# Kernel optimization log

Hardware: AMD Instinct MI355X
Metric: run time of the kernel (lower is better)

## Reference

```python
import jax, jax.numpy as jnp
import numpy as np

ALPHA = 0.2  # LeakyReLU negative slope


def setup_inputs() -> dict:
    key = jax.random.key(0)
    k1, k2, k3, k4 = jax.random.split(key, 4)
    B, N, Fin, Fout = 8, 2048, 256, 256
    h = jax.random.normal(k1, (B, N, Fin), dtype=jnp.float32)
    # random 0/1 adjacency with guaranteed self-loops so every row has a neighbor
    adj = jax.random.randint(k2, (N, N), 0, 2).astype(jnp.float32)
    adj = jnp.maximum(adj, jnp.eye(N, dtype=jnp.float32))
    # xavier_uniform with gain=1.414
    def xavier(k, shape, gain=1.414):
        fan_in, fan_out = shape[0], shape[1]
        a = gain * np.sqrt(6.0 / (fan_in + fan_out))
        return jax.random.uniform(k, shape, dtype=jnp.float32, minval=-a, maxval=a)
    W = xavier(k3, (Fin, Fout))
    a = xavier(k4, (2 * Fout, 1))
    return {"h": h, "adj_matrix": adj, "W": W, "a": a}


def reference(h, adj_matrix, W, a):
    # h: [B, N, Fin], adj_matrix: [N, N], W: [Fin, Fout], a: [2*Fout, 1]
    Fout = W.shape[1]
    Wh = jnp.einsum("bnf,fo->bno", h, W)            # [B, N, Fout]
    a1, a2 = a[:Fout, 0], a[Fout:, 0]                 # split additive attention vector
    # e[b,i,j] = leakyrelu(Wh[b,i]@a1 + Wh[b,j]@a2) — equals concat([Wh_i,Wh_j])@a
    s1 = Wh @ a1                                      # [B, N]
    s2 = Wh @ a2                                      # [B, N]
    e = s1[:, :, None] + s2[:, None, :]               # [B, N, N]
    e = jnp.where(e >= 0, e, ALPHA * e)               # LeakyReLU
    e = jnp.where(adj_matrix[None] == 0, -jnp.inf, e)  # mask non-edges
    attention = jax.nn.softmax(e, axis=-1)            # [B, N, N]
    # dropout is identity in eval mode (training=False)
    h_prime = jnp.einsum("bij,bjo->bio", attention, Wh)
    return h_prime
```

## Files before the change

### kernel.cpp

```cpp
#include <hip/hip_runtime.h>
#include <cstdint>

#define NN 2048
#define LOG2E 1.4426950408889634f

typedef __attribute__((ext_vector_type(8))) short bf16x8;
typedef __attribute__((ext_vector_type(4))) float f32x4;

__device__ __forceinline__ unsigned short f2bf(float x){
  union { float f; unsigned u; } v; v.f = x;
  unsigned r = v.u + 0x7FFFu + ((v.u >> 16) & 1u);
  return (unsigned short)(r >> 16);
}
__device__ __forceinline__ unsigned pack2(float a, float b){
  return (unsigned)f2bf(a) | ((unsigned)f2bf(b) << 16);
}
__device__ __forceinline__ unsigned permpack(unsigned hi, unsigned lo){
  return __builtin_amdgcn_perm(hi, lo, 0x07060302u);
}

__global__ __launch_bounds__(256) void k_prep(const float* __restrict__ adj,
                                              const float* __restrict__ W,
                                              unsigned long long* __restrict__ ab,
                                              unsigned short* __restrict__ Wt){
  const int tid = threadIdx.x;
  const int bid = blockIdx.x;
  if (bid < 512){
    const int lane = tid & 63;
    unsigned* ab32 = (unsigned*)ab;
    #pragma unroll
    for (int r = 0; r < 4; r++){
      const int row = bid * 4 + r;
      #pragma unroll
      for (int part = 0; part < 2; part++){
        float4 v = ((const float4*)(adj + (size_t)row * NN))[part * 256 + tid];
        unsigned n = (v.x != 0.f ? 1u : 0u) | (v.y != 0.f ? 2u : 0u)
                   | (v.z != 0.f ? 4u : 0u) | (v.w != 0.f ? 8u : 0u);
        unsigned m;
        m = __shfl_xor(n, 1); n = (lane & 1) ? (m | (n << 4))  : (n | (m << 4));
        m = __shfl_xor(n, 2); n = (lane & 2) ? (m | (n << 8))  : (n | (m << 8));
        m = __shfl_xor(n, 4); n = (lane & 4) ? (m | (n << 16)) : (n | (m << 16));
        if ((lane & 7) == 0)
          ab32[row * 64 + part * 32 + (tid >> 3)] = n;
      }
    }
  } else {
    int g = (bid - 512) * 256 + tid;
    int o = g >> 8, k = g & 255;
    Wt[g] = f2bf(W[k * 256 + o]);
  }
}

__global__ __launch_bounds__(512, 2) void k_fused_gemm(const float* __restrict__ h,
                                                       const unsigned short* __restrict__ Wt,
                                                       const float* __restrict__ a,
                                                       unsigned short* __restrict__ WhT,
                                                       float* __restrict__ s1c,
                                                       float* __restrict__ s2c){
  __shared__ __align__(16) unsigned char As[2 * 8192];
  __shared__ __align__(16) unsigned short Ts[256 * 72];
  __shared__ float s1p[8][64], s2p[8][64];
  const int tid = threadIdx.x;
  const int r0 = blockIdx.x * 64;
  const int b  = r0 >> 11;
  const int i0 = r0 & (NN - 1);
  const int w = tid >> 6, lane = tid & 63, lhi = lane >> 4, llo = lane & 15;
  const int wc = w * 32;
  const int sit = w >> 1, skk = w & 1;
  const int srow = sit * 16 + llo;
  const int skol = skk * 32 + lhi * 8;

  f32x4 acc[4][2];
  #pragma unroll
  for (int i = 0; i < 4; i++)
    #pragma unroll
    for (int j = 0; j < 2; j++){ acc[i][j][0]=0.f; acc[i][j][1]=0.f; acc[i][j][2]=0.f; acc[i][j][3]=0.f; }

  float4 hv[4][2];
  #pragma unroll
  for (int t = 0; t < 4; t++){
    const float* hp = h + (size_t)(r0 + srow) * 256 + t * 64 + skol;
    hv[t][0] = *(const float4*)hp;
    hv[t][1] = *(const float4*)(hp + 4);
  }

  auto loadB = [&](int k0, bf16x8* dst){
    #pragma unroll
    for (int ot = 0; ot < 2; ot++)
      #pragma unroll
      for (int kk = 0; kk < 2; kk++)
        dst[ot * 2 + kk] = *(const bf16x8*)(Wt + (size_t)(wc + ot * 16 + llo) * 256 + k0 + kk * 32 + lhi * 8);
  };
  bf16x8 bfr[2][4];
  loadB(0, bfr[0]);

  #pragma unroll
  for (int t = 0; t < 4; t++){
    uint4 q = make_uint4(pack2(hv[t][0].x, hv[t][0].y), pack2(hv[t][0].z, hv[t][0].w),
                         pack2(hv[t][1].x, hv[t][1].y), pack2(hv[t][1].z, hv[t][1].w));
    *(uint4*)&As[(t & 1) * 8192 + w * 1024 + lane * 16] = q;
    __syncthreads();
    if (t < 3) loadB((t + 1) * 64, bfr[(t + 1) & 1]);
    bf16x8 af[2][4];
    #pragma unroll
    for (int kk = 0; kk < 2; kk++)
      #pragma unroll
      for (int it = 0; it < 4; it++)
        af[kk][it] = *(const bf16x8*)&As[(t & 1) * 8192 + (it * 2 + kk) * 1024 + lane * 16];
    #pragma unroll
    for (int kk = 0; kk < 2; kk++)
      #pragma unroll
      for (int it = 0; it < 4; it++)
        #pragma unroll
        for (int ot = 0; ot < 2; ot++)
          acc[it][ot] = __builtin_amdgcn_mfma_f32_16x16x32_bf16(af[kk][it], bfr[t & 1][ot * 2 + kk], acc[it][ot], 0, 0, 0);
  }

  float a1v[2], a2v[2];
  #pragma unroll
  for (int ot = 0; ot < 2; ot++){
    a1v[ot] = a[wc + ot * 16 + llo] * LOG2E;
    a2v[ot] = a[256 + wc + ot * 16 + llo] * LOG2E;
  }
  #pragma unroll
  for (int it = 0; it < 4; it++){
    #pragma unroll
    for (int q = 0; q < 4; q++){
      float p1 = acc[it][0][q] * a1v[0] + acc[it][1][q] * a1v[1];
      float p2 = acc[it][0][q] * a2v[0] + acc[it][1][q] * a2v[1];
      #pragma unroll
      for (int o = 1; o < 16; o <<= 1){ p1 += __shfl_xor(p1, o); p2 += __shfl_xor(p2, o); }
      if (llo == 0){
        s1p[w][it * 16 + lhi * 4 + q] = p1;
        s2p[w][it * 16 + lhi * 4 + q] = p2;
      }
    }
  }

  #pragma unroll
  for (int it = 0; it < 4; it++){
    #pragma unroll
    for (int ot = 0; ot < 2; ot++){
      int o = wc + ot * 16 + llo;
      uint2 u = make_uint2(pack2(acc[it][ot][0], acc[it][ot][1]),
                           pack2(acc[it][ot][2], acc[it][ot][3]));
      *(uint2*)&Ts[o * 72 + it * 16 + lhi * 4] = u;
    }
  }
  __syncthreads();

  if (tid < 64){
    float t1 = 0.f, t2 = 0.f;
    #pragma unroll
    for (int g = 0; g < 8; g++){ t1 += s1p[g][tid]; t2 += s2p[g][tid]; }
    s1c[r0 + tid] = t1;
    s2c[r0 + tid] = t2;
  }
  #pragma unroll
  for (int p = 0; p < 4; p++){
    int o = p * 64 + (tid >> 3), col = (tid & 7) * 8;
    *(uint4*)(WhT + (size_t)(b * 256 + o) * 2048 + i0 + col) = *(const uint4*)&Ts[o * 72 + col];
  }
}

__global__ __launch_bounds__(512, 2) void k_attn(const float* __restrict__ s1c,
                                                 const float* __restrict__ s2c,
                                                 const unsigned short* __restrict__ WhT,
                                                 const unsigned long long* __restrict__ ab,
                                                 float* __restrict__ out){
  __shared__ __align__(16) float s2s[2048];
  __shared__ __align__(16) unsigned char PsB[2 * 16384];
  __shared__ __align__(16) unsigned char bitsB[64 * 264];
  __shared__ float s1s[64], lin[64], red[8], rsp[8][64];
  const int tid = threadIdx.x;
  const int bid = blockIdx.x;
  const int b = bid & 7, i0 = (bid >> 3) * 64;
  const int w = tid >> 6, lane = tid & 63, lhi = lane >> 4, llo = lane & 15;
  const int wc = w * 32;
  const int sit = w >> 1, skk = w & 1;
  const int sfrag = sit * 2 + skk;
  const int prow = sit * 16 + llo;

  float4 v = ((const float4*)(s2c + (size_t)b * NN))[tid];
  ((float4*)s2s)[tid] = v;
  float vmax = fmaxf(fmaxf(v.x, v.y), fmaxf(v.z, v.w));
  #pragma unroll
  for (int o = 32; o; o >>= 1) vmax = fmaxf(vmax, __shfl_xor(vmax, o));
  if (lane == 0) red[w] = vmax;
  if (tid < 64) s1s[tid] = s1c[(size_t)b * NN + i0 + tid];
  #pragma unroll
  for (int k = 0; k < 4; k++){
    int g = k * 512 + tid;
    unsigned long long mw = ab[(size_t)i0 * 32 + g];
    *(unsigned long long*)&bitsB[(g >> 5) * 264 + (g & 31) * 8] = mw;
  }
  __syncthreads();
  float m2 = red[0];
  #pragma unroll
  for (int g = 1; g < 8; g++) m2 = fmaxf(m2, red[g]);

  const float s1v = s1s[prow];
  const float xm = s1v + m2;
  const float mv = fmaxf(xm, 0.2f * xm);
  const float c1 = s1v - mv;
  const float c2 = 0.2f * s1v - mv;
  float rs = 0.f;

  f32x4 acc[4][2];
  #pragma unroll
  for (int i = 0; i < 4; i++)
    #pragma unroll
    for (int j = 0; j < 2; j++){ acc[i][j][0]=0.f; acc[i][j][1]=0.f; acc[i][j][2]=0.f; acc[i][j][3]=0.f; }

  auto loadB = [&](int j0, bf16x8* dst){
    #pragma unroll
    for (int jh = 0; jh < 2; jh++)
      #pragma unroll
      for (int ot = 0; ot < 2; ot++)
        #pragma unroll
        for (int kk = 0; kk < 2; kk++)
          dst[jh * 4 + ot * 2 + kk] = *(const bf16x8*)(WhT + (size_t)(b * 256 + wc + ot * 16 + llo) * 2048 + j0 + jh * 64 + kk * 32 + lhi * 8);
  };

  unsigned puq[8];
  auto computeP = [&](int tn, unsigned* pq){
    unsigned bits = bitsB[prow * 264 + tn * 8 + skk * 4 + lhi];
    const float* sp = &s2s[tn * 64 + skk * 32 + lhi * 8];
    float4 xa = *(const float4*)sp;
    float4 xb = *(const float4*)(sp + 4);
    float xs[8] = {xa.x, xa.y, xa.z, xa.w, xb.x, xb.y, xb.z, xb.w};
    unsigned pu[8];
    #pragma unroll
    for (int e = 0; e < 8; e++){
      float s2v = xs[e];
      float y = fmaxf(s2v + c1, __builtin_fmaf(0.2f, s2v, c2));
      float p = __builtin_amdgcn_exp2f(y);
      unsigned m = ((bits >> e) & 1u) ? 0xFFFF0000u : 0u;
      unsigned u = __float_as_uint(p) & m;
      rs += __uint_as_float(u);
      pu[e] = u;
    }
    pq[0] = permpack(pu[1], pu[0]); pq[1] = permpack(pu[3], pu[2]);
    pq[2] = permpack(pu[5], pu[4]); pq[3] = permpack(pu[7], pu[6]);
  };

  auto stageBody = [&](int t, int BUF, bf16x8* curB, bf16x8* nxtB, bool last){
    *(uint4*)&PsB[BUF * 16384 +        sfrag * 1024 + lane * 16] = *(uint4*)&puq[0];
    *(uint4*)&PsB[BUF * 16384 + 8192 + sfrag * 1024 + lane * 16] = *(uint4*)&puq[4];
    __syncthreads();
    if (!last) loadB((t + 1) * 128, nxtB);
    bf16x8 af[2][4];
    #pragma unroll
    for (int kk = 0; kk < 2; kk++)
      #pragma unroll
      for (int it = 0; it < 4; it++)
        af[kk][it] = *(const bf16x8*)&PsB[BUF * 16384 + (it * 2 + kk) * 1024 + lane * 16];
    if (!last) computeP(2 * (t + 1), &puq[0]);
    #pragma unroll
    for (int kk = 0; kk < 2; kk++)
      #pragma unroll
      for (int it = 0; it < 4; it++)
        #pragma unroll
        for (int ot = 0; ot < 2; ot++)
          acc[it][ot] = __builtin_amdgcn_mfma_f32_16x16x32_bf16(af[kk][it], curB[ot * 2 + kk], acc[it][ot], 0, 0, 0);
    #pragma unroll
    for (int kk = 0; kk < 2; kk++)
      #pragma unroll
      for (int it = 0; it < 4; it++)
        af[kk][it] = *(const bf16x8*)&PsB[BUF * 16384 + 8192 + (it * 2 + kk) * 1024 + lane * 16];
    if (!last) computeP(2 * (t + 1) + 1, &puq[4]);
    #pragma unroll
    for (int kk = 0; kk < 2; kk++)
      #pragma unroll
      for (int it = 0; it < 4; it++)
        #pragma unroll
        for (int ot = 0; ot < 2; ot++)
          acc[it][ot] = __builtin_amdgcn_mfma_f32_16x16x32_bf16(af[kk][it], curB[4 + ot * 2 + kk], acc[it][ot], 0, 0, 0);
  };

  bf16x8 bA[8], bB[8];
  loadB(0, bA);
  computeP(0, &puq[0]);
  computeP(1, &puq[4]);
  for (int t2 = 0; t2 < 16; t2 += 2){
    stageBody(t2,     0, bA, bB, false);
    stageBody(t2 + 1, 1, bB, bA, t2 + 1 == 15);
  }

  rs += __shfl_xor(rs, 16);
  rs += __shfl_xor(rs, 32);
  if (lhi == 0) rsp[w][prow] = rs;
  __syncthreads();
  if (tid < 64){
    int it = tid >> 4;
    lin[tid] = 1.0f / (rsp[it * 2][tid] + rsp[it * 2 + 1][tid]);
  }
  __syncthreads();

  #pragma unroll
  for (int it = 0; it < 4; it++){
    #pragma unroll
    for (int ot = 0; ot < 2; ot++){
      int col = wc + ot * 16 + llo;
      #pragma unroll
      for (int q = 0; q < 4; q++){
        int row = it * 16 + lhi * 4 + q;
        out[(size_t)(b * NN + i0 + row) * 256 + col] = acc[it][ot][q] * lin[row];
      }
    }
  }
}

extern "C" void kernel_launch(void* const* d_in, const int* in_sizes, int n_in,
                              void* d_out, int out_size, void* d_ws, size_t ws_size,
                              hipStream_t stream) {
  const float* h   = (const float*)d_in[0];
  const float* adj = (const float*)d_in[1];
  const float* W   = (const float*)d_in[2];
  const float* a   = (const float*)d_in[3];
  float* out = (float*)d_out;

  char* ws = (char*)d_ws;
  unsigned short* WhT      = (unsigned short*)(ws);
  unsigned short* Wt       = (unsigned short*)(ws + 8388608);
  unsigned long long* ab   = (unsigned long long*)(ws + 8519680);
  float* s1c               = (float*)(ws + 9043968);
  float* s2c               = (float*)(ws + 9109504);

  hipLaunchKernelGGL(k_prep,       dim3(768), dim3(256), 0, stream, adj, W, ab, Wt);
  hipLaunchKernelGGL(k_fused_gemm, dim3(256), dim3(512), 0, stream, h, Wt, a, WhT, s1c, s2c);
  hipLaunchKernelGGL(k_attn,       dim3(256), dim3(512), 0, stream, s1c, s2c, WhT, ab, out);
}
```

Before: 130.7 us.

## Split attention block across 16 waves, each owning 16 output columns

Doubles the k_attn block from 512 to 1024 threads. Each wave now owns a 16-column output slice instead of 32, and computes only one P fragment per stage instead of two. Row sums are reduced across four wave partials. This halves per-wave accumulator and B-register use and spreads the exp/mask work over more waves to raise latency hiding. In exchange, each wave issues more shared-memory A-fragment reads per MFMA, and barrier cost grows with more waves per block.

```diff
diff --git a/kernel.cpp b/kernel.cpp
--- a/kernel.cpp
+++ b/kernel.cpp
@@ -163,34 +163,35 @@
   }
 }
 
-__global__ __launch_bounds__(512, 2) void k_attn(const float* __restrict__ s1c,
-                                                 const float* __restrict__ s2c,
-                                                 const unsigned short* __restrict__ WhT,
-                                                 const unsigned long long* __restrict__ ab,
-                                                 float* __restrict__ out){
+__global__ __launch_bounds__(1024, 4) void k_attn(const float* __restrict__ s1c,
+                                                  const float* __restrict__ s2c,
+                                                  const unsigned short* __restrict__ WhT,
+                                                  const unsigned long long* __restrict__ ab,
+                                                  float* __restrict__ out){
   __shared__ __align__(16) float s2s[2048];
   __shared__ __align__(16) unsigned char PsB[2 * 16384];
   __shared__ __align__(16) unsigned char bitsB[64 * 264];
-  __shared__ float s1s[64], lin[64], red[8], rsp[8][64];
+  __shared__ float s1s[64], lin[64], red[8], rsp[16][64];
   const int tid = threadIdx.x;
   const int bid = blockIdx.x;
   const int b = bid & 7, i0 = (bid >> 3) * 64;
   const int w = tid >> 6, lane = tid & 63, lhi = lane >> 4, llo = lane & 15;
-  const int wc = w * 32;
-  const int sit = w >> 1, skk = w & 1;
-  const int sfrag = sit * 2 + skk;
-  const int prow = sit * 16 + llo;
-
-  float4 v = ((const float4*)(s2c + (size_t)b * NN))[tid];
-  ((float4*)s2s)[tid] = v;
-  float vmax = fmaxf(fmaxf(v.x, v.y), fmaxf(v.z, v.w));
-  #pragma unroll
-  for (int o = 32; o; o >>= 1) vmax = fmaxf(vmax, __shfl_xor(vmax, o));
-  if (lane == 0) red[w] = vmax;
+  const int wcol = w * 16;
+  const int jh = w >> 3, it = (w >> 1) & 3, kk = w & 1;
+  const int prow = it * 16 + llo;
+
+  if (tid < 512){
+    float4 v = ((const float4*)(s2c + (size_t)b * NN))[tid];
+    ((float4*)s2s)[tid] = v;
+    float vmax = fmaxf(fmaxf(v.x, v.y), fmaxf(v.z, v.w));
+    #pragma unroll
+    for (int o = 32; o; o >>= 1) vmax = fmaxf(vmax, __shfl_xor(vmax, o));
+    if (lane == 0) red[w] = vmax;
+  }
   if (tid < 64) s1s[tid] = s1c[(size_t)b * NN + i0 + tid];
   #pragma unroll
-  for (int k = 0; k < 4; k++){
-    int g = k * 512 + tid;
+  for (int k = 0; k < 2; k++){
+    int g = k * 1024 + tid;
     unsigned long long mw = ab[(size_t)i0 * 32 + g];
     *(unsigned long long*)&bitsB[(g >> 5) * 264 + (g & 31) * 8] = mw;
   }
@@ -206,26 +207,23 @@
   const float c2 = 0.2f * s1v - mv;
   float rs = 0.f;
 
-  f32x4 acc[4][2];
-  #pragma unroll
-  for (int i = 0; i < 4; i++)
-    #pragma unroll
-    for (int j = 0; j < 2; j++){ acc[i][j][0]=0.f; acc[i][j][1]=0.f; acc[i][j][2]=0.f; acc[i][j][3]=0.f; }
+  f32x4 acc[4];
+  #pragma unroll
+  for (int i = 0; i < 4; i++){ acc[i][0]=0.f; acc[i][1]=0.f; acc[i][2]=0.f; acc[i][3]=0.f; }
 
   auto loadB = [&](int j0, bf16x8* dst){
     #pragma unroll
-    for (int jh = 0; jh < 2; jh++)
-      #pragma unroll
-      for (int ot = 0; ot < 2; ot++)
-        #pragma unroll
-        for (int kk = 0; kk < 2; kk++)
-          dst[jh * 4 + ot * 2 + kk] = *(const bf16x8*)(WhT + (size_t)(b * 256 + wc + ot * 16 + llo) * 2048 + j0 + jh * 64 + kk * 32 + lhi * 8);
+    for (int jh2 = 0; jh2 < 2; jh2++)
+      #pragma unroll
+      for (int kk2 = 0; kk2 < 2; kk2++)
+        dst[jh2 * 2 + kk2] = *(const bf16x8*)(WhT + (size_t)(b * 256 + wcol + llo) * 2048 + j0 + jh2 * 64 + kk2 * 32 + lhi * 8);
   };
 
-  unsigned puq[8];
-  auto computeP = [&](int tn, unsigned* pq){
-    unsigned bits = bitsB[prow * 264 + tn * 8 + skk * 4 + lhi];
-    const float* sp = &s2s[tn * 64 + skk * 32 + lhi * 8];
+  unsigned puq[4];
+  auto computeP = [&](int t){
+    int tn = 2 * t + jh;
+    unsigned bits = bitsB[prow * 264 + tn * 8 + kk * 4 + lhi];
+    const float* sp = &s2s[tn * 64 + kk * 32 + lhi * 8];
     float4 xa = *(const float4*)sp;
     float4 xb = *(const float4*)(sp + 4);
     float xs[8] = {xa.x, xa.y, xa.z, xa.w, xb.x, xb.y, xb.z, xb.w};
@@ -240,48 +238,41 @@
       rs += __uint_as_float(u);
       pu[e] = u;
     }
-    pq[0] = permpack(pu[1], pu[0]); pq[1] = permpack(pu[3], pu[2]);
-    pq[2] = permpack(pu[5], pu[4]); pq[3] = permpack(pu[7], pu[6]);
+    puq[0] = permpack(pu[1], pu[0]); puq[1] = permpack(pu[3], pu[2]);
+    puq[2] = permpack(pu[5], pu[4]); puq[3] = permpack(pu[7], pu[6]);
   };
 
   auto stageBody = [&](int t, int BUF, bf16x8* curB, bf16x8* nxtB, bool last){
-    *(uint4*)&PsB[BUF * 16384 +        sfrag * 1024 + lane * 16] = *(uint4*)&puq[0];
-    *(uint4*)&PsB[BUF * 16384 + 8192 + sfrag * 1024 + lane * 16] = *(uint4*)&puq[4];
+    *(uint4*)&PsB[BUF * 16384 + w * 1024 + lane * 16] = *(uint4*)&puq[0];
     __syncthreads();
     if (!last) loadB((t + 1) * 128, nxtB);
     bf16x8 af[2][4];
     #pragma unroll
-    for (int kk = 0; kk < 2; kk++)
-      #pragma unroll
-      for (int it = 0; it < 4; it++)
-        af[kk][it] = *(const bf16x8*)&PsB[BUF * 16384 + (it * 2 + kk) * 1024 + lane * 16];
-    if (!last) computeP(2 * (t + 1), &puq[0]);
-    #pragma unroll
-    for (int kk = 0; kk < 2; kk++)
-      #pragma unroll
-      for (int it = 0; it < 4; it++)
-        #pragma unroll
-        for (int ot = 0; ot < 2; ot++)
-          acc[it][ot] = __builtin_amdgcn_mfma_f32_16x16x32_bf16(af[kk][it], curB[ot * 2 + kk], acc[it][ot], 0, 0, 0);
-    #pragma unroll
-    for (int kk = 0; kk < 2; kk++)
-      #pragma unroll
-      for (int it = 0; it < 4; it++)
-        af[kk][it] = *(const bf16x8*)&PsB[BUF * 16384 + 8192 + (it * 2 + kk) * 1024 + lane * 16];
-    if (!last) computeP(2 * (t + 1) + 1, &puq[4]);
-    #pragma unroll
-    for (int kk = 0; kk < 2; kk++)
-      #pragma unroll
-      for (int it = 0; it < 4; it++)
-        #pragma unroll
-        for (int ot = 0; ot < 2; ot++)
-          acc[it][ot] = __builtin_amdgcn_mfma_f32_16x16x32_bf16(af[kk][it], curB[4 + ot * 2 + kk], acc[it][ot], 0, 0, 0);
+    for (int kk2 = 0; kk2 < 2; kk2++)
+      #pragma unroll
+      for (int it2 = 0; it2 < 4; it2++)
+        af[kk2][it2] = *(const bf16x8*)&PsB[BUF * 16384 + (it2 * 2 + kk2) * 1024 + lane * 16];
+    if (!last) computeP(t + 1);
+    #pragma unroll
+    for (int kk2 = 0; kk2 < 2; kk2++)
+      #pragma unroll
+      for (int it2 = 0; it2 < 4; it2++)
+        acc[it2] = __builtin_amdgcn_mfma_f32_16x16x32_bf16(af[kk2][it2], curB[kk2], acc[it2], 0, 0, 0);
+    #pragma unroll
+    for (int kk2 = 0; kk2 < 2; kk2++)
+      #pragma unroll
+      for (int it2 = 0; it2 < 4; it2++)
+        af[kk2][it2] = *(const bf16x8*)&PsB[BUF * 16384 + 8192 + (it2 * 2 + kk2) * 1024 + lane * 16];
+    #pragma unroll
+    for (int kk2 = 0; kk2 < 2; kk2++)
+      #pragma unroll
+      for (int it2 = 0; it2 < 4; it2++)
+        acc[it2] = __builtin_amdgcn_mfma_f32_16x16x32_bf16(af[kk2][it2], curB[2 + kk2], acc[it2], 0, 0, 0);
   };
 
-  bf16x8 bA[8], bB[8];
+  bf16x8 bA[4], bB[4];
   loadB(0, bA);
-  computeP(0, &puq[0]);
-  computeP(1, &puq[4]);
+  computeP(0);
   for (int t2 = 0; t2 < 16; t2 += 2){
     stageBody(t2,     0, bA, bB, false);
     stageBody(t2 + 1, 1, bB, bA, t2 + 1 == 15);
@@ -292,21 +283,19 @@
   if (lhi == 0) rsp[w][prow] = rs;
   __syncthreads();
   if (tid < 64){
-    int it = tid >> 4;
-    lin[tid] = 1.0f / (rsp[it * 2][tid] + rsp[it * 2 + 1][tid]);
+    int rit = tid >> 4;
+    lin[tid] = 1.0f / (rsp[rit * 2][tid] + rsp[rit * 2 + 1][tid]
+                     + rsp[rit * 2 + 8][tid] + rsp[rit * 2 + 9][tid]);
   }
   __syncthreads();
 
   #pragma unroll
-  for (int it = 0; it < 4; it++){
-    #pragma unroll
-    for (int ot = 0; ot < 2; ot++){
-      int col = wc + ot * 16 + llo;
-      #pragma unroll
-      for (int q = 0; q < 4; q++){
-        int row = it * 16 + lhi * 4 + q;
-        out[(size_t)(b * NN + i0 + row) * 256 + col] = acc[it][ot][q] * lin[row];
-      }
+  for (int it2 = 0; it2 < 4; it2++){
+    int col = wcol + llo;
+    #pragma unroll
+    for (int q = 0; q < 4; q++){
+      int row = it2 * 16 + lhi * 4 + q;
+      out[(size_t)(b * NN + i0 + row) * 256 + col] = acc[it2][q] * lin[row];
     }
   }
 }
@@ -327,7 +316,7 @@
   float* s1c               = (float*)(ws + 9043968);
   float* s2c               = (float*)(ws + 9109504);
 
-  hipLaunchKernelGGL(k_prep,       dim3(768), dim3(256), 0, stream, adj, W, ab, Wt);
-  hipLaunchKernelGGL(k_fused_gemm, dim3(256), dim3(512), 0, stream, h, Wt, a, WhT, s1c, s2c);
-  hipLaunchKernelGGL(k_attn,       dim3(256), dim3(512), 0, stream, s1c, s2c, WhT, ab, out);
-}
+  hipLaunchKernelGGL(k_prep,       dim3(768), dim3(256),  0, stream, adj, W, ab, Wt);
+  hipLaunchKernelGGL(k_fused_gemm, dim3(256), dim3(512),  0, stream, h, Wt, a, WhT, s1c, s2c);
+  hipLaunchKernelGGL(k_attn,       dim3(256), dim3(1024), 0, stream, s1c, s2c, WhT, ab, out);
+}
```

After: 132.6 us. No clear change (+1.4%).
